# Kernel tuning notes

Measured on AMD Instinct MI355X. Metric: run time of the kernel, lower is better.

Reference implementation:

```python
import jax, jax.numpy as jnp
import numpy as np

B, P = 16, 1024
D_TIME, NUM_MODS = 8, 22
DIM_S = NUM_MODS + D_TIME + 1  # 31
PHI_W, N_HEADS, DP = 32, 4, 32
PSI_W, PSI_L, RHO_W = 64, 64, 64
SQRT_DP = float(np.sqrt(DP))


def setup_inputs() -> dict:
    key = jax.random.key(0)
    ks = jax.random.split(key, 16)
    rn = lambda k, shape: jax.random.normal(k, shape, jnp.float32) * 0.05
    return dict(
        times=jax.random.uniform(ks[0], (B, P), jnp.float32) * 48.0,
        values=jax.random.normal(ks[1], (B, P), jnp.float32),
        measurements=jax.random.randint(ks[2], (B, P), 0, NUM_MODS + 1),
        non_pad_mask=jnp.ones((B, P, 1), jnp.float32),
        W_psi1=rn(ks[3], (DIM_S, PSI_W)), b_psi1=jnp.zeros((PSI_W,), jnp.float32),
        W_psi2=rn(ks[4], (PSI_W, PSI_L)), b_psi2=jnp.zeros((PSI_L,), jnp.float32),
        W_key=rn(ks[5], (DIM_S + PSI_L, N_HEADS * DP)), b_key=jnp.zeros((N_HEADS * DP,), jnp.float32),
        query=rn(ks[6], (N_HEADS, DP)),
        W_phi1=rn(ks[7], (DIM_S, PHI_W)), b_phi1=jnp.zeros((PHI_W,), jnp.float32),
        W_phi2=rn(ks[8], (PHI_W, PHI_W)), b_phi2=jnp.zeros((PHI_W,), jnp.float32),
        W_rho1=rn(ks[9], (N_HEADS * PHI_W, RHO_W)), b_rho1=jnp.zeros((RHO_W,), jnp.float32),
        W_rho2=rn(ks[10], (RHO_W, RHO_W)), b_rho2=jnp.zeros((RHO_W,), jnp.float32),
    )


def _temporal_enc(times):
    i = np.arange(D_TIME)
    pos_vec = jnp.asarray(10000.0 ** (2.0 * (i // 2) / D_TIME), jnp.float32)
    ang = times[:, :, None] / pos_vec  # [B,P,d_time]
    return jnp.where(jnp.asarray(i % 2 == 0), jnp.sin(ang), jnp.cos(ang))


def reference(times, values, measurements, non_pad_mask,
              W_psi1, b_psi1, W_psi2, b_psi2, W_key, b_key, query,
              W_phi1, b_phi1, W_phi2, b_phi2, W_rho1, b_rho1, W_rho2, b_rho2):
    m = non_pad_mask  # [B,P,1]
    te = _temporal_enc(times)
    oh = jax.nn.one_hot(measurements, NUM_MODS + 1, dtype=jnp.float32)[:, :, 1:]
    x = jnp.concatenate([te, values[:, :, None], oh], axis=-1)  # [B,P,dim_s]

    # CumulativeSetAttentionLayer: psi MLP -> cumulative mean -> keys . query
    psi = jax.nn.relu(jax.nn.relu(x @ W_psi1 + b_psi1) @ W_psi2 + b_psi2)  # [B,P,psi_l]
    cum = jnp.cumsum(psi * m, axis=1) / jnp.cumsum(m, axis=1)
    keys = (jnp.concatenate([x, cum], axis=-1) @ W_key + b_key).reshape(B, P, N_HEADS, DP)
    pre = jnp.einsum('bpmd,md->bpm', keys, query) / SQRT_DP  # [B,P,m]

    # phi MLP
    phi = jax.nn.relu(jax.nn.relu(x @ W_phi1 + b_phi1) @ W_phi2 + b_phi2) * m  # [B,P,phi_w]

    # cumulative softmax weighting (online path)
    cmax = jax.lax.cummax(pre, axis=1)  # [B,P,m], running max for stability
    D = jnp.exp(pre[:, None, :, :] - cmax[:, :, None, :])  # [B,P,Q,m]
    causal = jnp.arange(P)[:, None] >= jnp.arange(P)[None, :]  # keep Q <= P
    D = D * causal[None, :, :, None]
    E = D.sum(axis=2)  # [B,P,m]
    agg = jnp.einsum('bpqm,bqd->bpmd', D, phi) / E[:, :, :, None]
    agg = (agg * m[:, :, :, None]).reshape(B, P, N_HEADS * PHI_W)

    # rho MLP (return_sequences)
    out = jax.nn.relu(jax.nn.relu(agg @ W_rho1 + b_rho1) @ W_rho2 + b_rho2) * m
    return out
```

## Files before the change

### kernel.cpp

```cpp
#include <hip/hip_runtime.h>
#include <hip/hip_bf16.h>

#define B_ 16
#define P_ 1024
#define T_ (B_*P_)
#define CH_ 16
#define CL_ (P_/CH_)

constexpr int OFF_A     = 16;
constexpr int OFF_TIMES = OFF_A     + 384;
constexpr int OFF_VALS  = OFF_TIMES + T_;
constexpr int OFF_MASK  = OFF_VALS  + T_;
constexpr int OFF_WPSI1 = OFF_MASK  + T_;
constexpr int OFF_BPSI1 = OFF_WPSI1 + 1984;
constexpr int OFF_WPSI2 = OFF_BPSI1 + 64;
constexpr int OFF_BPSI2 = OFF_WPSI2 + 4096;
constexpr int OFF_WKEY  = OFF_BPSI2 + 64;
constexpr int OFF_BKEY  = OFF_WKEY  + 12160;
constexpr int OFF_QRY   = OFF_BKEY  + 128;
constexpr int OFF_WPHI1 = OFF_QRY   + 128;
constexpr int OFF_BPHI1 = OFF_WPHI1 + 992;
constexpr int OFF_WPHI2 = OFF_BPHI1 + 32;
constexpr int OFF_BPHI2 = OFF_WPHI2 + 1024;
constexpr int OFF_WRHO1 = OFF_BPHI2 + 32;
constexpr int OFF_BRHO1 = OFF_WRHO1 + 8192;
constexpr int OFF_WRHO2 = OFF_BRHO1 + 64;
constexpr int OFF_BRHO2 = OFF_WRHO2 + 4096;
constexpr int OFF_PHI   = OFF_BRHO2 + 64;
constexpr int OFF_Z     = OFF_PHI   + T_*32;
constexpr int OFF_PREX  = OFF_Z     + T_*4;
constexpr int OFF_PRE   = OFF_PREX  + T_*4;
constexpr int OFF_AGG   = OFF_PRE   + T_*4;
constexpr int OFF_CME   = OFF_AGG   + T_*128;
constexpr int OFF_CS    = OFF_CME   + 2048;
constexpr int OFF_PME   = OFF_CS    + 32768;
constexpr int OFF_PS    = OFF_PME   + 2048;

static __device__ __forceinline__ bool detect_f32(const void* mask_raw) {
  return ((*(const unsigned*)mask_raw) & 0xFFFFu) == 0u;
}
static __device__ __forceinline__ float ld_any(const void* src, int i, bool isf32) {
  if (isf32) return ((const float*)src)[i];
  return __bfloat162float(((const __hip_bfloat16*)src)[i]);
}

__global__ __launch_bounds__(256) void s0_stage(
    float* __restrict__ ws,
    const void* times, const void* values, const void* mask,
    const void* Wpsi1, const void* bpsi1, const void* Wpsi2, const void* bpsi2,
    const void* Wkey,  const void* bkey,  const void* query,
    const void* Wphi1, const void* bphi1, const void* Wphi2, const void* bphi2,
    const void* Wrho1, const void* brho1, const void* Wrho2, const void* brho2) {
  const bool isf32 = detect_f32(mask);
  const int g  = blockIdx.x * 256 + threadIdx.x;
  const int gs = gridDim.x * 256;
  auto st = [&](int off, const void* src, int n) {
    for (int i = g; i < n; i += gs) ws[off + i] = ld_any(src, i, isf32);
  };
  st(OFF_TIMES, times, T_);   st(OFF_VALS, values, T_);  st(OFF_MASK, mask, T_);
  st(OFF_WPSI1, Wpsi1, 1984); st(OFF_BPSI1, bpsi1, 64);
  st(OFF_WPSI2, Wpsi2, 4096); st(OFF_BPSI2, bpsi2, 64);
  st(OFF_WKEY,  Wkey, 12160); st(OFF_BKEY,  bkey, 128);  st(OFF_QRY, query, 128);
  st(OFF_WPHI1, Wphi1, 992);  st(OFF_BPHI1, bphi1, 32);
  st(OFF_WPHI2, Wphi2, 1024); st(OFF_BPHI2, bphi2, 32);
  st(OFF_WRHO1, Wrho1, 8192); st(OFF_BRHO1, brho1, 64);
  st(OFF_WRHO2, Wrho2, 4096); st(OFF_BRHO2, brho2, 64);
}

__global__ __launch_bounds__(256) void s1_fold(float* __restrict__ ws) {
  const int gid = blockIdx.x * 256 + threadIdx.x;
  if (gid >= 384) return;
  const float inv_s = 0.17677669529663687f;
  const int h = gid & 3;
  const int j = gid >> 2;
  const float* src = (j < 95) ? (ws + OFF_WKEY + j * 128 + h * 32)
                              : (ws + OFF_BKEY + h * 32);
  const float* q = ws + OFF_QRY + h * 32;
  float s = 0.f;
  for (int d = 0; d < 32; ++d) s += src[d] * q[d];
  ws[OFF_A + gid] = s * inv_s;
}

__global__ __launch_bounds__(256) void k1_token(float* __restrict__ ws,
                                                const int* __restrict__ measp) {
  __shared__ float sh1[4][64];
  __shared__ float sg1[4][32];
  const int tid = threadIdx.x;
  const int wv  = __builtin_amdgcn_readfirstlane(tid >> 6);
  const int j   = tid & 63;
  const int t   = blockIdx.x * 4 + wv;

  const float tval = ws[OFF_TIMES + t];
  const float vval = ws[OFF_VALS + t];
  const float mval = ws[OFF_MASK + t];
  const int   meas = measp[t];
  const float sel  = (meas > 0) ? 1.f : 0.f;
  const int   mrow = (meas > 0) ? (8 + meas) : 0;

  float x[9];
  const float posv[4] = {1.f, 10.f, 100.f, 1000.f};
  #pragma unroll
  for (int k = 0; k < 4; ++k) {
    float s, c;
    __sincosf(tval / posv[k], &s, &c);
    x[2*k] = s; x[2*k+1] = c;
  }
  x[8] = vval;

  float h1 = ws[OFF_BPSI1 + j];
  #pragma unroll
  for (int i = 0; i < 9; ++i) h1 = fmaf(x[i], ws[OFF_WPSI1 + i * 64 + j], h1);
  h1 = fmaf(sel, ws[OFF_WPSI1 + mrow * 64 + j], h1);
  sh1[wv][j] = fmaxf(h1, 0.f);

  if (j < 32) {
    float g1 = ws[OFF_BPHI1 + j];
    #pragma unroll
    for (int i = 0; i < 9; ++i) g1 = fmaf(x[i], ws[OFF_WPHI1 + i * 32 + j], g1);
    g1 = fmaf(sel, ws[OFF_WPHI1 + mrow * 32 + j], g1);
    sg1[wv][j] = fmaxf(g1, 0.f);
  }
  __syncthreads();

  float h2 = ws[OFF_BPSI2 + j];
  #pragma unroll 8
  for (int i = 0; i < 64; ++i) h2 = fmaf(sh1[wv][i], ws[OFF_WPSI2 + i * 64 + j], h2);
  const float q = fmaxf(h2, 0.f) * mval;

  const float* a2 = ws + OFF_A + (31 + j) * 4;
  float z0 = q * a2[0], z1 = q * a2[1], z2 = q * a2[2], z3 = q * a2[3];
  #pragma unroll
  for (int off = 32; off; off >>= 1) {
    z0 += __shfl_xor(z0, off, 64);
    z1 += __shfl_xor(z1, off, 64);
    z2 += __shfl_xor(z2, off, 64);
    z3 += __shfl_xor(z3, off, 64);
  }
  if (j == 0) {
    float* zo = ws + OFF_Z + (size_t)t * 4;
    zo[0] = z0; zo[1] = z1; zo[2] = z2; zo[3] = z3;
  }

  if (j < 32) {
    float g2 = ws[OFF_BPHI2 + j];
    #pragma unroll 8
    for (int i = 0; i < 32; ++i) g2 = fmaf(sg1[wv][i], ws[OFF_WPHI2 + i * 32 + j], g2);
    ws[OFF_PHI + (size_t)t * 32 + j] = fmaxf(g2, 0.f) * mval;
  } else if (j < 36) {
    const int h = j - 32;
    float pr = ws[OFF_A + 380 + h];
    #pragma unroll
    for (int i = 0; i < 9; ++i) pr = fmaf(x[i], ws[OFF_A + i * 4 + h], pr);
    pr = fmaf(sel, ws[OFF_A + mrow * 4 + h], pr);
    ws[OFF_PREX + (size_t)t * 4 + h] = pr;
  }
}

__global__ __launch_bounds__(256) void k2_scanz(float* __restrict__ ws) {
  const int b   = blockIdx.x;
  const int tid = threadIdx.x;
  __shared__ float sc[256], s0[256], s1[256], s2[256], s3[256];

  const float* mB = ws + OFF_MASK + b * P_;
  const float* zB = ws + OFF_Z    + (size_t)b * P_ * 4;
  const int p0 = tid * 4;

  float lc[4], l0[4], l1[4], l2[4], l3[4];
  float c = 0.f, z0 = 0.f, z1 = 0.f, z2 = 0.f, z3 = 0.f;
  #pragma unroll
  for (int i = 0; i < 4; ++i) {
    c  += mB[p0 + i];
    z0 += zB[(p0 + i) * 4 + 0]; z1 += zB[(p0 + i) * 4 + 1];
    z2 += zB[(p0 + i) * 4 + 2]; z3 += zB[(p0 + i) * 4 + 3];
    lc[i] = c; l0[i] = z0; l1[i] = z1; l2[i] = z2; l3[i] = z3;
  }

  float rc = c, r0 = z0, r1 = z1, r2 = z2, r3 = z3;
  sc[tid] = rc; s0[tid] = r0; s1[tid] = r1; s2[tid] = r2; s3[tid] = r3;
  __syncthreads();
  for (int off = 1; off < 256; off <<= 1) {
    float ac = 0.f, a0 = 0.f, a1 = 0.f, a2 = 0.f, a3 = 0.f;
    if (tid >= off) {
      ac = sc[tid - off]; a0 = s0[tid - off]; a1 = s1[tid - off];
      a2 = s2[tid - off]; a3 = s3[tid - off];
    }
    __syncthreads();
    rc += ac; r0 += a0; r1 += a1; r2 += a2; r3 += a3;
    sc[tid] = rc; s0[tid] = r0; s1[tid] = r1; s2[tid] = r2; s3[tid] = r3;
    __syncthreads();
  }
  const float ec = rc - c, e0 = r0 - z0, e1 = r1 - z1, e2 = r2 - z2, e3 = r3 - z3;

  const float* px  = ws + OFF_PREX + (size_t)b * P_ * 4;
  float*       pre = ws + OFF_PRE  + (size_t)b * P_ * 4;
  #pragma unroll
  for (int i = 0; i < 4; ++i) {
    const float inv = 1.f / (ec + lc[i]);
    const int p = p0 + i;
    pre[p * 4 + 0] = px[p * 4 + 0] + (e0 + l0[i]) * inv;
    pre[p * 4 + 1] = px[p * 4 + 1] + (e1 + l1[i]) * inv;
    pre[p * 4 + 2] = px[p * 4 + 2] + (e2 + l2[i]) * inv;
    pre[p * 4 + 3] = px[p * 4 + 3] + (e3 + l3[i]) * inv;
  }
}

__global__ __launch_bounds__(128) void k4a_chunk(float* __restrict__ ws) {
  const int ch = blockIdx.x, b = blockIdx.y;
  const int h = threadIdx.x >> 5, d = threadIdx.x & 31;
  const float* preB = ws + OFF_PRE + (size_t)b * P_ * 4;
  const float* phiB = ws + OFF_PHI + (size_t)b * P_ * 32;

  float M = -__builtin_inff(), E = 0.f, S = 0.f;
  const int pbeg = ch * CL_;
  for (int p = pbeg; p < pbeg + CL_; ++p) {
    const float v  = preB[p * 4 + h];
    const float ph = phiB[p * 32 + d];
    const float nM = fmaxf(M, v);
    const float al = __expf(M - nM);
    const float w  = __expf(v - nM);
    E = fmaf(E, al, w);
    S = fmaf(S, al, w * ph);
    M = nM;
  }
  const int base = (b * CH_ + ch) * 4 + h;
  if (d == 0) { ws[OFF_CME + base * 2] = M; ws[OFF_CME + base * 2 + 1] = E; }
  ws[OFF_CS + base * 32 + d] = S;
}

__global__ __launch_bounds__(128) void k4b_prefix(float* __restrict__ ws) {
  const int b = blockIdx.x;
  const int h = threadIdx.x >> 5, d = threadIdx.x & 31;
  float M = -__builtin_inff(), E = 0.f, S = 0.f;
  for (int ch = 0; ch < CH_; ++ch) {
    const int base = (b * CH_ + ch) * 4 + h;
    if (d == 0) { ws[OFF_PME + base * 2] = M; ws[OFF_PME + base * 2 + 1] = E; }
    ws[OFF_PS + base * 32 + d] = S;
    const float cM = ws[OFF_CME + base * 2];
    const float cE = ws[OFF_CME + base * 2 + 1];
    const float cS = ws[OFF_CS  + base * 32 + d];
    const float nM = fmaxf(M, cM);
    const float a1 = __expf(M - nM);
    const float a2 = __expf(cM - nM);
    E = E * a1 + cE * a2;
    S = S * a1 + cS * a2;
    M = nM;
  }
}

__global__ __launch_bounds__(128) void k4c_replay(float* __restrict__ ws) {
  const int ch = blockIdx.x, b = blockIdx.y;
  const int h = threadIdx.x >> 5, d = threadIdx.x & 31;
  const float* preB = ws + OFF_PRE + (size_t)b * P_ * 4;
  const float* phiB = ws + OFF_PHI + (size_t)b * P_ * 32;
  const float* mB   = ws + OFF_MASK + b * P_;
  float*       aggB = ws + OFF_AGG + (size_t)b * P_ * 128;

  const int base = (b * CH_ + ch) * 4 + h;
  float M = ws[OFF_PME + base * 2];
  float E = ws[OFF_PME + base * 2 + 1];
  float S = ws[OFF_PS  + base * 32 + d];

  const int pbeg = ch * CL_;
  for (int p = pbeg; p < pbeg + CL_; ++p) {
    const float v  = preB[p * 4 + h];
    const float ph = phiB[p * 32 + d];
    const float nM = fmaxf(M, v);
    const float al = __expf(M - nM);
    const float w  = __expf(v - nM);
    E = fmaf(E, al, w);
    S = fmaf(S, al, w * ph);
    M = nM;
    aggB[p * 128 + h * 32 + d] = (S / E) * mB[p];
  }
}

__global__ __launch_bounds__(256) void k5_rho(const float* __restrict__ ws,
                                              const void* __restrict__ mask_raw,
                                              void* __restrict__ out) {
  __shared__ float sW1[128 * 64];
  __shared__ float sH1[16][64];
  const int tid = threadIdx.x;
  for (int i = tid; i < 128 * 64; i += 256) sW1[i] = ws[OFF_WRHO1 + i];

  const int wv = __builtin_amdgcn_readfirstlane(tid >> 6);
  const int j  = tid & 63;
  const int t0 = blockIdx.x * 16 + wv * 4;
  const float* aggB = ws + OFF_AGG;

  const float b1 = ws[OFF_BRHO1 + j];
  float a0 = b1, a1 = b1, a2 = b1, a3 = b1;
  __syncthreads();

  #pragma unroll 8
  for (int i = 0; i < 128; ++i) {
    const float w = sW1[i * 64 + j];
    a0 = fmaf(aggB[(size_t)(t0 + 0) * 128 + i], w, a0);
    a1 = fmaf(aggB[(size_t)(t0 + 1) * 128 + i], w, a1);
    a2 = fmaf(aggB[(size_t)(t0 + 2) * 128 + i], w, a2);
    a3 = fmaf(aggB[(size_t)(t0 + 3) * 128 + i], w, a3);
  }
  sH1[wv * 4 + 0][j] = fmaxf(a0, 0.f);
  sH1[wv * 4 + 1][j] = fmaxf(a1, 0.f);
  sH1[wv * 4 + 2][j] = fmaxf(a2, 0.f);
  sH1[wv * 4 + 3][j] = fmaxf(a3, 0.f);
  __syncthreads();

  const float b2 = ws[OFF_BRHO2 + j];
  float o0 = b2, o1 = b2, o2 = b2, o3 = b2;
  #pragma unroll 8
  for (int i = 0; i < 64; ++i) {
    const float w = ws[OFF_WRHO2 + i * 64 + j];
    o0 = fmaf(sH1[wv * 4 + 0][i], w, o0);
    o1 = fmaf(sH1[wv * 4 + 1][i], w, o1);
    o2 = fmaf(sH1[wv * 4 + 2][i], w, o2);
    o3 = fmaf(sH1[wv * 4 + 3][i], w, o3);
  }

  const bool isf32 = detect_f32(mask_raw);
  float r[4] = {o0, o1, o2, o3};
  #pragma unroll
  for (int k = 0; k < 4; ++k) {
    const int t = t0 + k;
    const float v = fmaxf(r[k], 0.f) * ws[OFF_MASK + t];
    if (isf32) {
      ((float*)out)[(size_t)t * 64 + j] = v;
    } else {
      __hip_bfloat16 bb = __float2bfloat16(v);
      ((__hip_bfloat16*)out)[(size_t)t * 64 + j] = bb;
    }
  }
}

extern "C" void kernel_launch(void* const* d_in, const int* in_sizes, int n_in,
                              void* d_out, int out_size, void* d_ws, size_t ws_size,
                              hipStream_t stream) {
  const int* meas = (const int*)d_in[2];
  const void* mask = d_in[3];
  float* ws = (float*)d_ws;

  s0_stage<<<96, 256, 0, stream>>>(ws, d_in[0], d_in[1], mask,
                                   d_in[4], d_in[5], d_in[6], d_in[7],
                                   d_in[8], d_in[9], d_in[10],
                                   d_in[11], d_in[12], d_in[13], d_in[14],
                                   d_in[15], d_in[16], d_in[17], d_in[18]);
  s1_fold<<<2, 256, 0, stream>>>(ws);
  k1_token<<<T_/4, 256, 0, stream>>>(ws, meas);
  k2_scanz<<<B_, 256, 0, stream>>>(ws);
  k4a_chunk<<<dim3(CH_, B_), 128, 0, stream>>>(ws);
  k4b_prefix<<<B_, 128, 0, stream>>>(ws);
  k4c_replay<<<dim3(CH_, B_), 128, 0, stream>>>(ws);
  k5_rho<<<T_/16, 256, 0, stream>>>(ws, mask, d_out);
}
```

Measured before the change: 170.8 us.

## Fuse staging and fold kernels, read inputs directly, merge prefix into replay

The staging and key-query folding kernels are merged into one launch. The per-token times, values and mask are no longer copied into the workspace; kernels read them straight from the inputs with dtype detection. The serial prefix kernel is removed, and each replay block instead recomputes its own cross-chunk prefix from the chunk summaries. The chunk count doubles to give the scan kernels more parallelism. Together these cut two launches and some memory traffic, at the cost of redundant prefix work in later chunks.

```diff
diff --git a/kernel.cpp b/kernel.cpp
--- a/kernel.cpp
+++ b/kernel.cpp
@@ -4,14 +4,11 @@
 #define B_ 16
 #define P_ 1024
 #define T_ (B_*P_)
-#define CH_ 16
+#define CH_ 32
 #define CL_ (P_/CH_)
 
 constexpr int OFF_A     = 16;
-constexpr int OFF_TIMES = OFF_A     + 384;
-constexpr int OFF_VALS  = OFF_TIMES + T_;
-constexpr int OFF_MASK  = OFF_VALS  + T_;
-constexpr int OFF_WPSI1 = OFF_MASK  + T_;
+constexpr int OFF_WPSI1 = 400;
 constexpr int OFF_BPSI1 = OFF_WPSI1 + 1984;
 constexpr int OFF_WPSI2 = OFF_BPSI1 + 64;
 constexpr int OFF_BPSI2 = OFF_WPSI2 + 4096;
@@ -32,9 +29,7 @@
 constexpr int OFF_PRE   = OFF_PREX  + T_*4;
 constexpr int OFF_AGG   = OFF_PRE   + T_*4;
 constexpr int OFF_CME   = OFF_AGG   + T_*128;
-constexpr int OFF_CS    = OFF_CME   + 2048;
-constexpr int OFF_PME   = OFF_CS    + 32768;
-constexpr int OFF_PS    = OFF_PME   + 2048;
+constexpr int OFF_CS    = OFF_CME   + 4096;
 
 static __device__ __forceinline__ bool detect_f32(const void* mask_raw) {
   return ((*(const unsigned*)mask_raw) & 0xFFFFu) == 0u;
@@ -44,55 +39,59 @@
   return __bfloat162float(((const __hip_bfloat16*)src)[i]);
 }
 
-__global__ __launch_bounds__(256) void s0_stage(
-    float* __restrict__ ws,
-    const void* times, const void* values, const void* mask,
+__global__ __launch_bounds__(256) void s01_prep(
+    float* __restrict__ ws, const void* mask,
     const void* Wpsi1, const void* bpsi1, const void* Wpsi2, const void* bpsi2,
     const void* Wkey,  const void* bkey,  const void* query,
     const void* Wphi1, const void* bphi1, const void* Wphi2, const void* bphi2,
     const void* Wrho1, const void* brho1, const void* Wrho2, const void* brho2) {
   const bool isf32 = detect_f32(mask);
-  const int g  = blockIdx.x * 256 + threadIdx.x;
-  const int gs = gridDim.x * 256;
+  if (blockIdx.x < 2) {
+    const int gid = blockIdx.x * 256 + threadIdx.x;
+    if (gid >= 384) return;
+    const float inv_s = 0.17677669529663687f;
+    const int h = gid & 3;
+    const int j = gid >> 2;
+    float s = 0.f;
+    if (j < 95) {
+      for (int d = 0; d < 32; ++d)
+        s += ld_any(Wkey, j * 128 + h * 32 + d, isf32) * ld_any(query, h * 32 + d, isf32);
+    } else {
+      for (int d = 0; d < 32; ++d)
+        s += ld_any(bkey, h * 32 + d, isf32) * ld_any(query, h * 32 + d, isf32);
+    }
+    ws[OFF_A + gid] = s * inv_s;
+    return;
+  }
+  const int g  = (blockIdx.x - 2) * 256 + threadIdx.x;
+  const int gs = (gridDim.x - 2) * 256;
   auto st = [&](int off, const void* src, int n) {
     for (int i = g; i < n; i += gs) ws[off + i] = ld_any(src, i, isf32);
   };
-  st(OFF_TIMES, times, T_);   st(OFF_VALS, values, T_);  st(OFF_MASK, mask, T_);
   st(OFF_WPSI1, Wpsi1, 1984); st(OFF_BPSI1, bpsi1, 64);
   st(OFF_WPSI2, Wpsi2, 4096); st(OFF_BPSI2, bpsi2, 64);
-  st(OFF_WKEY,  Wkey, 12160); st(OFF_BKEY,  bkey, 128);  st(OFF_QRY, query, 128);
   st(OFF_WPHI1, Wphi1, 992);  st(OFF_BPHI1, bphi1, 32);
   st(OFF_WPHI2, Wphi2, 1024); st(OFF_BPHI2, bphi2, 32);
   st(OFF_WRHO1, Wrho1, 8192); st(OFF_BRHO1, brho1, 64);
   st(OFF_WRHO2, Wrho2, 4096); st(OFF_BRHO2, brho2, 64);
 }
 
-__global__ __launch_bounds__(256) void s1_fold(float* __restrict__ ws) {
-  const int gid = blockIdx.x * 256 + threadIdx.x;
-  if (gid >= 384) return;
-  const float inv_s = 0.17677669529663687f;
-  const int h = gid & 3;
-  const int j = gid >> 2;
-  const float* src = (j < 95) ? (ws + OFF_WKEY + j * 128 + h * 32)
-                              : (ws + OFF_BKEY + h * 32);
-  const float* q = ws + OFF_QRY + h * 32;
-  float s = 0.f;
-  for (int d = 0; d < 32; ++d) s += src[d] * q[d];
-  ws[OFF_A + gid] = s * inv_s;
-}
-
 __global__ __launch_bounds__(256) void k1_token(float* __restrict__ ws,
-                                                const int* __restrict__ measp) {
+                                                const int* __restrict__ measp,
+                                                const void* __restrict__ times,
+                                                const void* __restrict__ values,
+                                                const void* __restrict__ mask) {
   __shared__ float sh1[4][64];
   __shared__ float sg1[4][32];
+  const bool isf32 = detect_f32(mask);
   const int tid = threadIdx.x;
   const int wv  = __builtin_amdgcn_readfirstlane(tid >> 6);
   const int j   = tid & 63;
   const int t   = blockIdx.x * 4 + wv;
 
-  const float tval = ws[OFF_TIMES + t];
-  const float vval = ws[OFF_VALS + t];
-  const float mval = ws[OFF_MASK + t];
+  const float tval = ld_any(times, t, isf32);
+  const float vval = ld_any(values, t, isf32);
+  const float mval = ld_any(mask, t, isf32);
   const int   meas = measp[t];
   const float sel  = (meas > 0) ? 1.f : 0.f;
   const int   mrow = (meas > 0) ? (8 + meas) : 0;
@@ -156,20 +155,21 @@
   }
 }
 
-__global__ __launch_bounds__(256) void k2_scanz(float* __restrict__ ws) {
+__global__ __launch_bounds__(256) void k2_scanz(float* __restrict__ ws,
+                                                const void* __restrict__ mask) {
   const int b   = blockIdx.x;
   const int tid = threadIdx.x;
+  const bool isf32 = detect_f32(mask);
   __shared__ float sc[256], s0[256], s1[256], s2[256], s3[256];
 
-  const float* mB = ws + OFF_MASK + b * P_;
-  const float* zB = ws + OFF_Z    + (size_t)b * P_ * 4;
+  const float* zB = ws + OFF_Z + (size_t)b * P_ * 4;
   const int p0 = tid * 4;
 
   float lc[4], l0[4], l1[4], l2[4], l3[4];
   float c = 0.f, z0 = 0.f, z1 = 0.f, z2 = 0.f, z3 = 0.f;
   #pragma unroll
   for (int i = 0; i < 4; ++i) {
-    c  += mB[p0 + i];
+    c  += ld_any(mask, b * P_ + p0 + i, isf32);
     z0 += zB[(p0 + i) * 4 + 0]; z1 += zB[(p0 + i) * 4 + 1];
     z2 += zB[(p0 + i) * 4 + 2]; z3 += zB[(p0 + i) * 4 + 3];
     lc[i] = c; l0[i] = z0; l1[i] = z1; l2[i] = z2; l3[i] = z3;
@@ -227,17 +227,21 @@
   ws[OFF_CS + base * 32 + d] = S;
 }
 
-__global__ __launch_bounds__(128) void k4b_prefix(float* __restrict__ ws) {
-  const int b = blockIdx.x;
+__global__ __launch_bounds__(128) void k4c_replay(float* __restrict__ ws,
+                                                  const void* __restrict__ mask) {
+  const int ch = blockIdx.x, b = blockIdx.y;
   const int h = threadIdx.x >> 5, d = threadIdx.x & 31;
+  const bool isf32 = detect_f32(mask);
+  const float* preB = ws + OFF_PRE + (size_t)b * P_ * 4;
+  const float* phiB = ws + OFF_PHI + (size_t)b * P_ * 32;
+  float*       aggB = ws + OFF_AGG + (size_t)b * P_ * 128;
+
   float M = -__builtin_inff(), E = 0.f, S = 0.f;
-  for (int ch = 0; ch < CH_; ++ch) {
-    const int base = (b * CH_ + ch) * 4 + h;
-    if (d == 0) { ws[OFF_PME + base * 2] = M; ws[OFF_PME + base * 2 + 1] = E; }
-    ws[OFF_PS + base * 32 + d] = S;
-    const float cM = ws[OFF_CME + base * 2];
-    const float cE = ws[OFF_CME + base * 2 + 1];
-    const float cS = ws[OFF_CS  + base * 32 + d];
+  for (int c2 = 0; c2 < ch; ++c2) {
+    const int base2 = (b * CH_ + c2) * 4 + h;
+    const float cM = ws[OFF_CME + base2 * 2];
+    const float cE = ws[OFF_CME + base2 * 2 + 1];
+    const float cS = ws[OFF_CS  + base2 * 32 + d];
     const float nM = fmaxf(M, cM);
     const float a1 = __expf(M - nM);
     const float a2 = __expf(cM - nM);
@@ -245,20 +249,6 @@
     S = S * a1 + cS * a2;
     M = nM;
   }
-}
-
-__global__ __launch_bounds__(128) void k4c_replay(float* __restrict__ ws) {
-  const int ch = blockIdx.x, b = blockIdx.y;
-  const int h = threadIdx.x >> 5, d = threadIdx.x & 31;
-  const float* preB = ws + OFF_PRE + (size_t)b * P_ * 4;
-  const float* phiB = ws + OFF_PHI + (size_t)b * P_ * 32;
-  const float* mB   = ws + OFF_MASK + b * P_;
-  float*       aggB = ws + OFF_AGG + (size_t)b * P_ * 128;
-
-  const int base = (b * CH_ + ch) * 4 + h;
-  float M = ws[OFF_PME + base * 2];
-  float E = ws[OFF_PME + base * 2 + 1];
-  float S = ws[OFF_PS  + base * 32 + d];
 
   const int pbeg = ch * CL_;
   for (int p = pbeg; p < pbeg + CL_; ++p) {
@@ -270,7 +260,7 @@
     E = fmaf(E, al, w);
     S = fmaf(S, al, w * ph);
     M = nM;
-    aggB[p * 128 + h * 32 + d] = (S / E) * mB[p];
+    aggB[p * 128 + h * 32 + d] = (S / E) * ld_any(mask, b * P_ + p, isf32);
   }
 }
 
@@ -321,7 +311,7 @@
   #pragma unroll
   for (int k = 0; k < 4; ++k) {
     const int t = t0 + k;
-    const float v = fmaxf(r[k], 0.f) * ws[OFF_MASK + t];
+    const float v = fmaxf(r[k], 0.f) * ld_any(mask_raw, t, isf32);
     if (isf32) {
       ((float*)out)[(size_t)t * 64 + j] = v;
     } else {
@@ -335,19 +325,19 @@
                               void* d_out, int out_size, void* d_ws, size_t ws_size,
                               hipStream_t stream) {
   const int* meas = (const int*)d_in[2];
+  const void* times = d_in[0];
+  const void* values = d_in[1];
   const void* mask = d_in[3];
   float* ws = (float*)d_ws;
 
-  s0_stage<<<96, 256, 0, stream>>>(ws, d_in[0], d_in[1], mask,
+  s01_prep<<<34, 256, 0, stream>>>(ws, mask,
                                    d_in[4], d_in[5], d_in[6], d_in[7],
                                    d_in[8], d_in[9], d_in[10],
                                    d_in[11], d_in[12], d_in[13], d_in[14],
                                    d_in[15], d_in[16], d_in[17], d_in[18]);
-  s1_fold<<<2, 256, 0, stream>>>(ws);
-  k1_token<<<T_/4, 256, 0, stream>>>(ws, meas);
-  k2_scanz<<<B_, 256, 0, stream>>>(ws);
+  k1_token<<<T_/4, 256, 0, stream>>>(ws, meas, times, values, mask);
+  k2_scanz<<<B_, 256, 0, stream>>>(ws, mask);
   k4a_chunk<<<dim3(CH_, B_), 128, 0, stream>>>(ws);
-  k4b_prefix<<<B_, 128, 0, stream>>>(ws);
-  k4c_replay<<<dim3(CH_, B_), 128, 0, stream>>>(ws);
+  k4c_replay<<<dim3(CH_, B_), 128, 0, stream>>>(ws, mask);
   k5_rho<<<T_/16, 256, 0, stream>>>(ws, mask, d_out);
 }
```

New measurement: 162.5 us. 4.9% less time.
